# Kernel optimization log

Hardware: AMD Instinct MI355X
Metric: run time of the kernel (lower is better)

The kernel has to match this reference:

```python
import jax, jax.numpy as jnp
import numpy as np

BATCH, FIELDS, DIM = 1024, 39, 32
L0_OUT, L1_OUT = 256, 128  # cin_layer_size


def setup_inputs() -> dict:
    key = jax.random.key(0)
    ks = jax.random.split(key, 5)
    x = jax.random.normal(ks[0], (BATCH, FIELDS, DIM), dtype=jnp.float32)
    # Conv1d(kernel_size=1) weights stored as (out_channels, in_channels)
    w0 = jax.random.normal(ks[1], (L0_OUT, FIELDS * FIELDS), dtype=jnp.float32) * 0.02
    b0 = jax.random.normal(ks[2], (L0_OUT,), dtype=jnp.float32) * 0.02
    w1 = jax.random.normal(ks[3], (L1_OUT, FIELDS * (L0_OUT // 2)), dtype=jnp.float32) * 0.02
    b1 = jax.random.normal(ks[4], (L1_OUT,), dtype=jnp.float32) * 0.02
    return {"x": x, "w0": w0, "b0": b0, "w1": w1, "b1": b1}


def _cin_layer(x0, h_prev, w, b):
    # outer product over field axes at each embedding position, then 1x1 conv (= GEMM over channels)
    bsz, m, d = x0.shape
    z = jnp.einsum('bmd,bnd->bmnd', x0, h_prev).reshape(bsz, m * h_prev.shape[1], d)
    return jax.nn.relu(jnp.einsum('bid,oi->bod', z, w) + b[None, :, None])


def reference(x, w0, b0, w1, b1):
    # Layer 0: cross x with itself -> (B, m*m, D) -> conv -> relu
    h0 = _cin_layer(x, x, w0, b0)            # (B, 256, D)
    h1a, h1b = jnp.split(h0, 2, axis=1)      # each (B, 128, D); h1a feeds next layer
    # Layer 1 (final): cross x with h1a
    h1 = _cin_layer(x, h1a, w1, b1)          # (B, 128, D)
    # sum-pool over embedding dim of concatenated hidden outputs (hidden_layer[1:])
    return jnp.sum(jnp.concatenate([h1b, h1], axis=1), axis=-1)  # (B, 256)
```

## Files before the change

### kernel.cpp

```cpp
#include <hip/hip_runtime.h>


typedef _Float16 f16x8 __attribute__((ext_vector_type(8)));
typedef float f32x4 __attribute__((ext_vector_type(4)));

#define NB 2
#define NBLK 512
#define THREADS 512
#define K0P 52
#define M1C 40
#define M1P 42

__global__ __launch_bounds__(256) void prep_kernel(
    const float* __restrict__ w0, const float* __restrict__ w1,
    _Float16* __restrict__ w0c, _Float16* __restrict__ w1c) {
  int stride = gridDim.x * blockDim.x;
  int tid = blockIdx.x * blockDim.x + threadIdx.x;
  const int n0 = K0P * 8192;
  for (int idx = tid; idx < n0; idx += stride) {
    int j = idx & 7, lhi = (idx >> 3) & 3, l15 = (idx >> 5) & 15;
    int mt = (idx >> 9) & 1, w8 = (idx >> 10) & 7, s = idx >> 13;
    int o = w8 * 32 + mt * 16 + l15;
    int ip = s * 32 + lhi * 8 + j;
    float v = 0.f;
    if (ip < 1600) {
      int c5 = ip / 320;
      int m = (ip - c5 * 320) >> 3;
      int n = c5 * 8 + (ip & 7);
      if (m < 39 && n < 39) v = w0[o * 1521 + m * 39 + n];
    }
    w0c[idx] = (_Float16)v;
  }
  const int n1 = M1P * 16384;
  for (int idx = tid; idx < n1; idx += stride) {
    int j = idx & 7, lhi = (idx >> 3) & 3, l15 = (idx >> 5) & 15;
    int mt = (idx >> 9) & 1, kf = (idx >> 10) & 1, rt = (idx >> 11) & 3;
    int kh = (idx >> 13) & 1, m = idx >> 14;
    int o = rt * 32 + mt * 16 + l15;
    int k = kh * 64 + kf * 32 + lhi * 8 + j;
    float v = (m < 39) ? w1[o * 4992 + m * 128 + k] : 0.f;
    w1c[idx] = (_Float16)v;
  }
}

__global__ __launch_bounds__(512, 2) void cin_kernel(
    const float* __restrict__ x,
    const _Float16* __restrict__ w0c, const float* __restrict__ b0,
    const _Float16* __restrict__ w1c, const float* __restrict__ b1,
    float* __restrict__ out) {
  __shared__ __align__(16) _Float16 xs[NB * 32 * 40];
  __shared__ __align__(16) _Float16 h1[NB * 32 * 136];
  __shared__ __align__(16) float red[4 * 32 * 65];

  const int t = threadIdx.x;
  const int bb = blockIdx.x * NB;
  const int w = t >> 6;
  const int l15 = t & 15;
  const int lhi = (t >> 4) & 3;
  const int lane_off = ((l15 << 2) | lhi) << 3;

  int xrow[4];
#pragma unroll
  for (int nt = 0; nt < 4; ++nt) xrow[nt] = (nt * 16 + l15) * 40;

  for (int idx = t; idx < NB * 39 * 32; idx += THREADS) {
    int b = idx / 1248; int rem = idx - b * 1248;
    int m = rem >> 5; int d = rem & 31;
    xs[(b * 32 + d) * 40 + m] = (_Float16)x[(bb + b) * 1248 + rem];
  }
  if (t < NB * 32) xs[t * 40 + 39] = (_Float16)0.f;
  __syncthreads();

  f32x4 acc[2][4] = {};
  const _Float16* p0 = w0c + w * 1024 + lane_off;

  f16x8 af[2][2];
  f16x8 ck[2][4];
  _Float16 xmr[2][4];

  auto loadA0 = [&](int s, int b) {
    const _Float16* p = p0 + s * 8192;
    af[b][0] = *(const f16x8*)(p);
    af[b][1] = *(const f16x8*)(p + 512);
  };
  auto loadCk = [&](int g, int b) {
#pragma unroll
    for (int nt = 0; nt < 4; ++nt)
      ck[b][nt] = *(const f16x8*)&xs[xrow[nt] + g * 8];
  };
  auto xmld = [&](int s, int b) {
    int m = 4 * (s % 10) + lhi;
#pragma unroll
    for (int nt = 0; nt < 4; ++nt) xmr[b][nt] = xs[xrow[nt] + m];
  };

  loadCk(0, 0);
  xmld(0, 0);
  loadA0(0, 0); loadA0(1, 1);
#pragma unroll
  for (int s = 0; s < 50; ++s) {
    const int g = s / 10;
    if (s + 1 < 50) xmld(s + 1, (s + 1) & 1);
    if ((s % 10) == 0 && g + 1 < 5) loadCk(g + 1, (g + 1) & 1);
    f16x8 bz[4];
#pragma unroll
    for (int nt = 0; nt < 4; ++nt) bz[nt] = ck[g & 1][nt] * xmr[s & 1][nt];
#pragma unroll
    for (int mt = 0; mt < 2; ++mt)
#pragma unroll
      for (int nt = 0; nt < 4; ++nt)
        acc[mt][nt] = __builtin_amdgcn_mfma_f32_16x16x32_f16(af[s & 1][mt], bz[nt], acc[mt][nt], 0, 0, 0);
    if (s + 2 <= 51) loadA0(s + 2, s & 1);
  }

  if (w < 4) {
#pragma unroll
    for (int mt = 0; mt < 2; ++mt) {
#pragma unroll
      for (int nt = 0; nt < 4; ++nt) {
        int c = nt * 16 + l15;
        int hbase = c * 136;
#pragma unroll
        for (int r = 0; r < 4; ++r) {
          int o = w * 32 + mt * 16 + lhi * 4 + r;
          float v = fmaxf(acc[mt][nt][r] + b0[o], 0.f);
          h1[hbase + o] = (_Float16)v;
        }
      }
    }
  } else {
#pragma unroll
    for (int mt = 0; mt < 2; ++mt) {
#pragma unroll
      for (int r = 0; r < 4; ++r) {
        int o = w * 32 + mt * 16 + lhi * 4 + r;
        float bias = b0[o];
        float sb0 = 0.f, sb1 = 0.f;
#pragma unroll
        for (int nt = 0; nt < 4; ++nt) {
          float v = fmaxf(acc[mt][nt][r] + bias, 0.f);
          v += __shfl_xor(v, 1); v += __shfl_xor(v, 2);
          v += __shfl_xor(v, 4); v += __shfl_xor(v, 8);
          if (nt < 2) sb0 += v; else sb1 += v;
        }
        if (l15 == 0) {
          out[(bb + 0) * 256 + (o - 128)] = sb0;
          out[(bb + 1) * 256 + (o - 128)] = sb1;
        }
      }
    }
  }
  __syncthreads();

  const int rt = w >> 1;
  const int kh = w & 1;

  f16x8 hf[2][4];
#pragma unroll
  for (int kf = 0; kf < 2; ++kf)
#pragma unroll
    for (int nt = 0; nt < 4; ++nt)
      hf[kf][nt] = *(const f16x8*)&h1[(nt * 16 + l15) * 136 + (kh * 2 + kf) * 32 + lhi * 8];

  f32x4 acc2[2][4] = {};
  const _Float16* p1 = w1c + (kh * 4 + rt) * 2048 + lane_off;

  float xmv[2][4];
  auto xmvld = [&](int m, int b) {
#pragma unroll
    for (int nt = 0; nt < 4; ++nt) xmv[b][nt] = (float)xs[xrow[nt] + m];
  };
  auto loadA1 = [&](int m, f16x8 (&wf)[2][2]) {
    const _Float16* p = p1 + m * 16384;
    wf[0][0] = *(const f16x8*)(p);
    wf[0][1] = *(const f16x8*)(p + 512);
    wf[1][0] = *(const f16x8*)(p + 1024);
    wf[1][1] = *(const f16x8*)(p + 1536);
  };
  auto computeM = [&](int m, f16x8 (&wf)[2][2], float (&xv)[4]) {
#pragma unroll
    for (int mt = 0; mt < 2; ++mt)
#pragma unroll
      for (int nt = 0; nt < 4; ++nt) {
        f32x4 Y = __builtin_amdgcn_mfma_f32_16x16x32_f16(wf[0][mt], hf[0][nt],
                                                         (f32x4){0.f, 0.f, 0.f, 0.f}, 0, 0, 0);
        Y = __builtin_amdgcn_mfma_f32_16x16x32_f16(wf[1][mt], hf[1][nt], Y, 0, 0, 0);
        acc2[mt][nt] += Y * xv[nt];
      }
  };

  {
    f16x8 wfA[2][2], wfB[2][2];
    loadA1(0, wfA);
    loadA1(1, wfB);
    xmvld(0, 0);
    for (int m = 0; m < M1C; m += 2) {
      xmvld(m + 1, 1);
      computeM(m, wfA, xmv[0]);     loadA1(m + 2, wfA);
      if (m + 2 < M1C) xmvld(m + 2, 0);
      computeM(m + 1, wfB, xmv[1]); loadA1(m + 3, wfB);
    }
  }

  __syncthreads();
  if (kh == 1) {
#pragma unroll
    for (int mt = 0; mt < 2; ++mt)
#pragma unroll
      for (int nt = 0; nt < 4; ++nt)
#pragma unroll
        for (int r = 0; r < 4; ++r) {
          int row = mt * 16 + lhi * 4 + r, c = nt * 16 + l15;
          red[(rt * 32 + row) * 65 + c] = acc2[mt][nt][r];
        }
  }
  __syncthreads();
  if (kh == 0) {
#pragma unroll
    for (int mt = 0; mt < 2; ++mt)
#pragma unroll
      for (int nt = 0; nt < 4; ++nt)
#pragma unroll
        for (int r = 0; r < 4; ++r) {
          int row = mt * 16 + lhi * 4 + r, c = nt * 16 + l15;
          acc2[mt][nt][r] += red[(rt * 32 + row) * 65 + c];
        }

#pragma unroll
    for (int mt = 0; mt < 2; ++mt) {
#pragma unroll
      for (int r = 0; r < 4; ++r) {
        int o = rt * 32 + mt * 16 + lhi * 4 + r;
        float bias = b1[o];
        float sb0 = 0.f, sb1 = 0.f;
#pragma unroll
        for (int nt = 0; nt < 4; ++nt) {
          float v = fmaxf(acc2[mt][nt][r] + bias, 0.f);
          v += __shfl_xor(v, 1); v += __shfl_xor(v, 2);
          v += __shfl_xor(v, 4); v += __shfl_xor(v, 8);
          if (nt < 2) sb0 += v; else sb1 += v;
        }
        if (l15 == 0) {
          out[(bb + 0) * 256 + 128 + o] = sb0;
          out[(bb + 1) * 256 + 128 + o] = sb1;
        }
      }
    }
  }
}

extern "C" void kernel_launch(void* const* d_in, const int* in_sizes, int n_in,
                              void* d_out, int out_size, void* d_ws, size_t ws_size,
                              hipStream_t stream) {
  const float* x  = (const float*)d_in[0];
  const float* w0 = (const float*)d_in[1];
  const float* b0 = (const float*)d_in[2];
  const float* w1 = (const float*)d_in[3];
  const float* b1 = (const float*)d_in[4];
  float* out = (float*)d_out;

  _Float16* w0c = (_Float16*)d_ws;
  _Float16* w1c = w0c + K0P * 8192;

  prep_kernel<<<256, 256, 0, stream>>>(w0, w1, w0c, w1c);
  cin_kernel<<<NBLK, THREADS, 0, stream>>>(x, w0c, b0, w1c, b1, out);
}
```

Measured before the change: 91.42 us.

## Retile layer-0 MFMA GEMM into 64-row by 32-column warp tiles with register-cached x

Layer 0 is retiled so each warp computes a 64x32 output tile (4 row MFMA tiles by 2 column tiles) instead of 32x64, with the packed w0 layout regenerated to match. The x column fragments for all five n-blocks are loaded from shared memory into registers once, which removes the per-group shared-memory reloads. The change halves the number of Hadamard products per MFMA and reduces LDS traffic. In exchange each warp holds more weight fragments in registers, which could raise register pressure under the 2-blocks-per-CU launch bound.

```diff
diff --git a/kernel.cpp b/kernel.cpp
--- a/kernel.cpp
+++ b/kernel.cpp
@@ -8,28 +8,25 @@
 #define NBLK 512
 #define THREADS 512
 #define K0P 52
-#define M1C 40
 #define M1P 42
 
 __global__ __launch_bounds__(256) void prep_kernel(
     const float* __restrict__ w0, const float* __restrict__ w1,
-    _Float16* __restrict__ w0c, _Float16* __restrict__ w1c) {
+    _Float16* __restrict__ w0n, _Float16* __restrict__ w1c) {
   int stride = gridDim.x * blockDim.x;
   int tid = blockIdx.x * blockDim.x + threadIdx.x;
   const int n0 = K0P * 8192;
   for (int idx = tid; idx < n0; idx += stride) {
     int j = idx & 7, lhi = (idx >> 3) & 3, l15 = (idx >> 5) & 15;
-    int mt = (idx >> 9) & 1, w8 = (idx >> 10) & 7, s = idx >> 13;
-    int o = w8 * 32 + mt * 16 + l15;
-    int ip = s * 32 + lhi * 8 + j;
+    int mt = (idx >> 9) & 3, rg = (idx >> 11) & 3, s = idx >> 13;
+    int o = rg * 64 + mt * 16 + l15;
     float v = 0.f;
-    if (ip < 1600) {
-      int c5 = ip / 320;
-      int m = (ip - c5 * 320) >> 3;
-      int n = c5 * 8 + (ip & 7);
+    if (s < 50) {
+      int nbi = s / 10, mg = s - nbi * 10;
+      int m = mg * 4 + lhi, n = nbi * 8 + j;
       if (m < 39 && n < 39) v = w0[o * 1521 + m * 39 + n];
     }
-    w0c[idx] = (_Float16)v;
+    w0n[idx] = (_Float16)v;
   }
   const int n1 = M1P * 16384;
   for (int idx = tid; idx < n1; idx += stride) {
@@ -45,11 +42,11 @@
 
 __global__ __launch_bounds__(512, 2) void cin_kernel(
     const float* __restrict__ x,
-    const _Float16* __restrict__ w0c, const float* __restrict__ b0,
+    const _Float16* __restrict__ w0n, const float* __restrict__ b0,
     const _Float16* __restrict__ w1c, const float* __restrict__ b1,
     float* __restrict__ out) {
   __shared__ __align__(16) _Float16 xs[NB * 32 * 40];
-  __shared__ __align__(16) _Float16 h1[NB * 32 * 136];
+  __shared__ __align__(16) _Float16 h1[64 * 136];
   __shared__ __align__(16) float red[4 * 32 * 65];
 
   const int t = threadIdx.x;
@@ -57,11 +54,7 @@
   const int w = t >> 6;
   const int l15 = t & 15;
   const int lhi = (t >> 4) & 3;
-  const int lane_off = ((l15 << 2) | lhi) << 3;
-
-  int xrow[4];
-#pragma unroll
-  for (int nt = 0; nt < 4; ++nt) xrow[nt] = (nt * 16 + l15) * 40;
+  const int lane_off = l15 * 32 + lhi * 8;
 
   for (int idx = t; idx < NB * 39 * 32; idx += THREADS) {
     int b = idx / 1248; int rem = idx - b * 1248;
@@ -71,89 +64,95 @@
   if (t < NB * 32) xs[t * 40 + 39] = (_Float16)0.f;
   __syncthreads();
 
-  f32x4 acc[2][4] = {};
-  const _Float16* p0 = w0c + w * 1024 + lane_off;
-
-  f16x8 af[2][2];
-  f16x8 ck[2][4];
-  _Float16 xmr[2][4];
-
+  const int rg = w >> 1, cg = w & 1;
+  const int xc0 = (cg * 32 + l15) * 40;
+  const int xc1 = (cg * 32 + 16 + l15) * 40;
+
+  f16x8 xreg[2][5];
+#pragma unroll
+  for (int q = 0; q < 5; ++q) {
+    xreg[0][q] = *(const f16x8*)&xs[xc0 + q * 8];
+    xreg[1][q] = *(const f16x8*)&xs[xc1 + q * 8];
+  }
+
+  f32x4 acc[4][2] = {};
+  const _Float16* p0 = w0n + rg * 2048 + lane_off;
+  f16x8 af[2][4];
   auto loadA0 = [&](int s, int b) {
     const _Float16* p = p0 + s * 8192;
-    af[b][0] = *(const f16x8*)(p);
-    af[b][1] = *(const f16x8*)(p + 512);
-  };
-  auto loadCk = [&](int g, int b) {
-#pragma unroll
-    for (int nt = 0; nt < 4; ++nt)
-      ck[b][nt] = *(const f16x8*)&xs[xrow[nt] + g * 8];
-  };
-  auto xmld = [&](int s, int b) {
-    int m = 4 * (s % 10) + lhi;
-#pragma unroll
-    for (int nt = 0; nt < 4; ++nt) xmr[b][nt] = xs[xrow[nt] + m];
-  };
-
-  loadCk(0, 0);
+#pragma unroll
+    for (int mt = 0; mt < 4; ++mt) af[b][mt] = *(const f16x8*)(p + mt * 512);
+  };
+  _Float16 xmr[2][2];
+  auto xmld = [&](int mg4, int b) {
+    xmr[b][0] = xs[xc0 + mg4 + lhi];
+    xmr[b][1] = xs[xc1 + mg4 + lhi];
+  };
+
+  loadA0(0, 0); loadA0(1, 1);
   xmld(0, 0);
-  loadA0(0, 0); loadA0(1, 1);
-#pragma unroll
-  for (int s = 0; s < 50; ++s) {
-    const int g = s / 10;
-    if (s + 1 < 50) xmld(s + 1, (s + 1) & 1);
-    if ((s % 10) == 0 && g + 1 < 5) loadCk(g + 1, (g + 1) & 1);
-    f16x8 bz[4];
-#pragma unroll
-    for (int nt = 0; nt < 4; ++nt) bz[nt] = ck[g & 1][nt] * xmr[s & 1][nt];
-#pragma unroll
-    for (int mt = 0; mt < 2; ++mt)
-#pragma unroll
-      for (int nt = 0; nt < 4; ++nt)
-        acc[mt][nt] = __builtin_amdgcn_mfma_f32_16x16x32_f16(af[s & 1][mt], bz[nt], acc[mt][nt], 0, 0, 0);
-    if (s + 2 <= 51) loadA0(s + 2, s & 1);
-  }
-
-  if (w < 4) {
-#pragma unroll
-    for (int mt = 0; mt < 2; ++mt) {
-#pragma unroll
-      for (int nt = 0; nt < 4; ++nt) {
-        int c = nt * 16 + l15;
-        int hbase = c * 136;
+#pragma unroll
+  for (int nbi = 0; nbi < 5; ++nbi) {
+    for (int mg2 = 0; mg2 < 5; ++mg2) {
+      const int s = nbi * 10 + mg2 * 2;
+      xmld((mg2 * 2 + 1) * 4, 1);
+      {
+        f16x8 bz0 = xreg[0][nbi] * xmr[0][0];
+        f16x8 bz1 = xreg[1][nbi] * xmr[0][1];
+#pragma unroll
+        for (int mt = 0; mt < 4; ++mt) {
+          acc[mt][0] = __builtin_amdgcn_mfma_f32_16x16x32_f16(af[0][mt], bz0, acc[mt][0], 0, 0, 0);
+          acc[mt][1] = __builtin_amdgcn_mfma_f32_16x16x32_f16(af[0][mt], bz1, acc[mt][1], 0, 0, 0);
+        }
+      }
+      loadA0(s + 2, 0);
+      if (s + 2 < 50) xmld(mg2 < 4 ? (mg2 * 2 + 2) * 4 : 0, 0);
+      {
+        f16x8 bz0 = xreg[0][nbi] * xmr[1][0];
+        f16x8 bz1 = xreg[1][nbi] * xmr[1][1];
+#pragma unroll
+        for (int mt = 0; mt < 4; ++mt) {
+          acc[mt][0] = __builtin_amdgcn_mfma_f32_16x16x32_f16(af[1][mt], bz0, acc[mt][0], 0, 0, 0);
+          acc[mt][1] = __builtin_amdgcn_mfma_f32_16x16x32_f16(af[1][mt], bz1, acc[mt][1], 0, 0, 0);
+        }
+      }
+      loadA0(s + 3, 1);
+    }
+  }
+
+  if (rg < 2) {
+#pragma unroll
+    for (int mt = 0; mt < 4; ++mt)
+#pragma unroll
+      for (int nt = 0; nt < 2; ++nt) {
+        int c = cg * 32 + nt * 16 + l15;
 #pragma unroll
         for (int r = 0; r < 4; ++r) {
-          int o = w * 32 + mt * 16 + lhi * 4 + r;
+          int o = rg * 64 + mt * 16 + lhi * 4 + r;
           float v = fmaxf(acc[mt][nt][r] + b0[o], 0.f);
-          h1[hbase + o] = (_Float16)v;
-        }
-      }
-    }
+          h1[c * 136 + o] = (_Float16)v;
+        }
+      }
   } else {
 #pragma unroll
-    for (int mt = 0; mt < 2; ++mt) {
+    for (int mt = 0; mt < 4; ++mt)
 #pragma unroll
       for (int r = 0; r < 4; ++r) {
-        int o = w * 32 + mt * 16 + lhi * 4 + r;
+        int o = rg * 64 + mt * 16 + lhi * 4 + r;
         float bias = b0[o];
-        float sb0 = 0.f, sb1 = 0.f;
-#pragma unroll
-        for (int nt = 0; nt < 4; ++nt) {
-          float v = fmaxf(acc[mt][nt][r] + bias, 0.f);
-          v += __shfl_xor(v, 1); v += __shfl_xor(v, 2);
-          v += __shfl_xor(v, 4); v += __shfl_xor(v, 8);
-          if (nt < 2) sb0 += v; else sb1 += v;
-        }
-        if (l15 == 0) {
-          out[(bb + 0) * 256 + (o - 128)] = sb0;
-          out[(bb + 1) * 256 + (o - 128)] = sb1;
-        }
-      }
-    }
+        float v = fmaxf(acc[mt][0][r] + bias, 0.f) + fmaxf(acc[mt][1][r] + bias, 0.f);
+        v += __shfl_xor(v, 1); v += __shfl_xor(v, 2);
+        v += __shfl_xor(v, 4); v += __shfl_xor(v, 8);
+        if (l15 == 0) out[(bb + cg) * 256 + (o - 128)] = v;
+      }
   }
   __syncthreads();
 
   const int rt = w >> 1;
   const int kh = w & 1;
+  int xrow4[4];
+#pragma unroll
+  for (int nt = 0; nt < 4; ++nt) xrow4[nt] = (nt * 16 + l15) * 40;
 
   f16x8 hf[2][4];
 #pragma unroll
@@ -168,7 +167,7 @@
   float xmv[2][4];
   auto xmvld = [&](int m, int b) {
 #pragma unroll
-    for (int nt = 0; nt < 4; ++nt) xmv[b][nt] = (float)xs[xrow[nt] + m];
+    for (int nt = 0; nt < 4; ++nt) xmv[b][nt] = (float)xs[xrow4[nt] + m];
   };
   auto loadA1 = [&](int m, f16x8 (&wf)[2][2]) {
     const _Float16* p = p1 + m * 16384;
@@ -177,7 +176,7 @@
     wf[1][0] = *(const f16x8*)(p + 1024);
     wf[1][1] = *(const f16x8*)(p + 1536);
   };
-  auto computeM = [&](int m, f16x8 (&wf)[2][2], float (&xv)[4]) {
+  auto computeM = [&](f16x8 (&wf)[2][2], float (&xv)[4]) {
 #pragma unroll
     for (int mt = 0; mt < 2; ++mt)
 #pragma unroll
@@ -194,11 +193,11 @@
     loadA1(0, wfA);
     loadA1(1, wfB);
     xmvld(0, 0);
-    for (int m = 0; m < M1C; m += 2) {
+    for (int m = 0; m < 40; m += 2) {
       xmvld(m + 1, 1);
-      computeM(m, wfA, xmv[0]);     loadA1(m + 2, wfA);
-      if (m + 2 < M1C) xmvld(m + 2, 0);
-      computeM(m + 1, wfB, xmv[1]); loadA1(m + 3, wfB);
+      computeM(wfA, xmv[0]);     loadA1(m + 2, wfA);
+      if (m + 2 < 40) xmvld(m + 2, 0);
+      computeM(wfB, xmv[1]);     loadA1(m + 3, wfB);
     }
   }
 
@@ -259,9 +258,9 @@
   const float* b1 = (const float*)d_in[4];
   float* out = (float*)d_out;
 
-  _Float16* w0c = (_Float16*)d_ws;
-  _Float16* w1c = w0c + K0P * 8192;
-
-  prep_kernel<<<256, 256, 0, stream>>>(w0, w1, w0c, w1c);
-  cin_kernel<<<NBLK, THREADS, 0, stream>>>(x, w0c, b0, w1c, b1, out);
+  _Float16* w0n = (_Float16*)d_ws;
+  _Float16* w1c = w0n + K0P * 8192;
+
+  prep_kernel<<<256, 256, 0, stream>>>(w0, w1, w0n, w1c);
+  cin_kernel<<<NBLK, THREADS, 0, stream>>>(x, w0n, b0, w1c, b1, out);
 }
```

New measurement: 117.9 us. 28.9% more time.
